# Optimization experiments

Measured on AMD Instinct MI355X. Metric: run time of the kernel, lower is better.

The kernel has to match this reference:

```python
import jax, jax.numpy as jnp
import numpy as np

ALPHA = 1.702  # gpt-oss gated-activation alpha
LIMIT = 7.0    # gpt-oss clamp limit
E, H, I = 8, 1024, 2048
B, S = 2, 2048


def setup_inputs() -> dict:
    key = jax.random.key(0)
    ks = jax.random.split(key, 6)
    return {
        "hidden_states": jax.random.normal(ks[0], (B, S, H), dtype=jnp.float32),
        "routing_weights": jax.random.uniform(ks[1], (B * S, E), dtype=jnp.float32),
        "gate_up_proj": jax.random.normal(ks[2], (E, H, 2 * I), dtype=jnp.float32) * 0.02,
        "gate_up_proj_bias": jax.random.normal(ks[3], (E, 2 * I), dtype=jnp.float32) * 0.02,
        "down_proj": jax.random.normal(ks[4], (E, I, H), dtype=jnp.float32) * 0.02,
        "down_proj_bias": jax.random.normal(ks[5], (E, H), dtype=jnp.float32) * 0.02,
    }


def reference(hidden_states, routing_weights, gate_up_proj, gate_up_proj_bias,
              down_proj, down_proj_bias):
    b, s, h = hidden_states.shape
    x = hidden_states.reshape(-1, h)  # [T, H]
    # all-experts dense path: [E, T, 2I]
    gate_up = jnp.einsum('th,ehd->etd', x, gate_up_proj) + gate_up_proj_bias[:, None, :]
    gate = gate_up[..., ::2]   # interleaved gate/up as in gpt-oss
    up = gate_up[..., 1::2]
    gate = jnp.minimum(gate, LIMIT)
    up = jnp.clip(up, -LIMIT, LIMIT)
    glu = gate * jax.nn.sigmoid(gate * ALPHA)
    # [E, T, H]
    out_e = jnp.einsum('eti,eih->eth', (up + 1.0) * glu, down_proj) + down_proj_bias[:, None, :]
    # weighted sum over experts with routing weights [T, E]
    out = jnp.einsum('eth,te->th', out_e, routing_weights)
    return out.reshape(b, s, h)
```

## Files before the change

### kernel.cpp

```cpp
#include <hip/hip_runtime.h>
#include <cstdint>

#define E_  8
#define H_  1024
#define I_  2048
#define T_  4096
#define D2_ 4096
#define K2_ 16384

typedef __bf16 bf16x8 __attribute__((ext_vector_type(8)));
typedef float  f32x4  __attribute__((ext_vector_type(4)));

__device__ __forceinline__ unsigned short f2bf(float f) {
  unsigned int u = __float_as_uint(f);
  u += 0x7FFFu + ((u >> 16) & 1u);
  return (unsigned short)(u >> 16);
}

__device__ __forceinline__ void gll16(const void* g, void* l) {
  __builtin_amdgcn_global_load_lds(
      (const __attribute__((address_space(1))) unsigned int*)(uintptr_t)g,
      (__attribute__((address_space(3))) unsigned int*)(uintptr_t)l,
      16, 0, 0);
}

#define BARX()  __builtin_amdgcn_s_barrier()
#define FENCE() __builtin_amdgcn_sched_barrier(0)
#define WLG()   { asm volatile("s_waitcnt lgkmcnt(0)" ::: "memory"); __builtin_amdgcn_sched_barrier(0); }
#define LGK0()  asm volatile("s_waitcnt lgkmcnt(0)" ::: "memory")
#define WVM4()  asm volatile("s_waitcnt vmcnt(4)" ::: "memory")
#define WVM0()  asm volatile("s_waitcnt vmcnt(0)" ::: "memory")

__global__ void cast_x_kernel(const float* __restrict__ x,
                              unsigned short* __restrict__ xb) {
  const int idx = (blockIdx.x * 256 + threadIdx.x) * 8;
  float4 a = *(const float4*)(x + idx);
  float4 b = *(const float4*)(x + idx + 4);
  unsigned short o[8];
  o[0]=f2bf(a.x); o[1]=f2bf(a.y); o[2]=f2bf(a.z); o[3]=f2bf(a.w);
  o[4]=f2bf(b.x); o[5]=f2bf(b.y); o[6]=f2bf(b.z); o[7]=f2bf(b.w);
  *(uint4*)(xb + idx) = *(const uint4*)o;
}

__global__ void transp_w1_kernel(const float* __restrict__ gup,
                                 unsigned short* __restrict__ w1g,
                                 unsigned short* __restrict__ w1u) {
  __shared__ float tile[64][65];
  const int h0 = blockIdx.x * 64;
  const int d0 = blockIdx.y * 64;
  const int e  = blockIdx.z;
  const int tid = threadIdx.x;
  const int r  = tid >> 4;
  const int c4 = (tid & 15) * 4;
  const float* src = gup + ((size_t)e * H_ + h0) * D2_ + d0;
#pragma unroll
  for (int c = 0; c < 4; ++c) {
    const int row = r + 16 * c;
    float4 v = *(const float4*)(src + (size_t)row * D2_ + c4);
    tile[row][c4+0] = v.x; tile[row][c4+1] = v.y;
    tile[row][c4+2] = v.z; tile[row][c4+3] = v.w;
  }
  __syncthreads();
  const int hl = tid & 63;
  const int jg = tid >> 6;
  const size_t jbase = (size_t)e * I_ + (d0 >> 1);
#pragma unroll
  for (int jj = 0; jj < 8; ++jj) {
    const int jl = jg * 8 + jj;
    w1g[(jbase + jl) * H_ + h0 + hl] = f2bf(tile[hl][2*jl]);
    w1u[(jbase + jl) * H_ + h0 + hl] = f2bf(tile[hl][2*jl+1]);
  }
}

__global__ void transp_w2_kernel(const float* __restrict__ dp,
                                 unsigned short* __restrict__ w2t) {
  __shared__ float tile[64][65];
  const int k0 = blockIdx.x * 64;
  const int h0 = blockIdx.y * 64;
  const int tid = threadIdx.x;
  const int r  = tid >> 4;
  const int c4 = (tid & 15) * 4;
#pragma unroll
  for (int c = 0; c < 4; ++c) {
    const int row = r + 16 * c;
    float4 v = *(const float4*)(dp + (size_t)(k0 + row) * H_ + h0 + c4);
    tile[row][c4+0] = v.x; tile[row][c4+1] = v.y;
    tile[row][c4+2] = v.z; tile[row][c4+3] = v.w;
  }
  __syncthreads();
  const int kl = tid & 63;
  const int hg = tid >> 6;
#pragma unroll
  for (int hh = 0; hh < 16; ++hh) {
    const int hl = hg * 16 + hh;
    w2t[(size_t)(h0 + hl) * K2_ + k0 + kl] = f2bf(tile[kl][hl]);
  }
}


#define STA1(B, HF, KT) {                                                    \
  _Pragma("unroll")                                                           \
  for (int ld = 0; ld < 2; ++ld) {                                            \
    const int r = rA + (HF)*64 + ld*128;                                      \
    gll16(Ag + (size_t)r * H_ + (KT)*64 + sg, &lds[B][r*64 + sl]);            \
  } }
#define STG1(B, KT) {                                                         \
  _Pragma("unroll")                                                           \
  for (int ld = 0; ld < 2; ++ld) {                                            \
    const int r = rA + ld*64;                                                 \
    gll16(Gg + (size_t)r * H_ + (KT)*64 + sg, &lds[B][16384 + r*64 + sl]);    \
  } }
#define STU1(B, KT) {                                                         \
  _Pragma("unroll")                                                           \
  for (int ld = 0; ld < 2; ++ld) {                                            \
    const int r = rA + ld*64;                                                 \
    gll16(Ug + (size_t)r * H_ + (KT)*64 + sg, &lds[B][24576 + r*64 + sl]);    \
  } }
#define LDA1(B, MH) {                                                         \
  _Pragma("unroll")                                                           \
  for (int m = 0; m < 4; ++m) {                                               \
    const int ro = (wm*128 + (MH)*64 + m*16 + arow) * 64;                     \
    av[m][0] = *(const bf16x8*)&lds[B][ro + sw0];                             \
    av[m][1] = *(const bf16x8*)&lds[B][ro + sw1];                             \
  } }
#define LDB1(B, DST, BASE) {                                                  \
  _Pragma("unroll")                                                           \
  for (int n = 0; n < 2; ++n) {                                               \
    const int ro = (BASE) + (wn*32 + n*16 + arow) * 64;                       \
    DST[n][0] = *(const bf16x8*)&lds[B][ro + sw0];                            \
    DST[n][1] = *(const bf16x8*)&lds[B][ro + sw1];                            \
  } }
#define MMA1(ACC, MH, BV)                                                     \
  __builtin_amdgcn_s_setprio(1);                                              \
  _Pragma("unroll")                                                           \
  for (int m = 0; m < 4; ++m)                                                 \
  _Pragma("unroll")                                                           \
  for (int n = 0; n < 2; ++n) {                                               \
    ACC[(MH)*4+m][n] = __builtin_amdgcn_mfma_f32_16x16x32_bf16(av[m][0], BV[n][0], ACC[(MH)*4+m][n], 0,0,0); \
    ACC[(MH)*4+m][n] = __builtin_amdgcn_mfma_f32_16x16x32_bf16(av[m][1], BV[n][1], ACC[(MH)*4+m][n], 0,0,0); \
  }                                                                           \
  __builtin_amdgcn_s_setprio(0);

#define NT1 16
#define TILE1(B, U) {                                                         \
    \
  LDA1(B, 0); LDB1(B, bgv, 16384); LDB1(B, buv, 24576);                       \
  if ((U)+1 < NT1) { STA1((B)^1, 1, (U)+1); STG1((B)^1, (U)+1); }             \
  WLG();                                                                      \
  MMA1(accg, 0, bgv); MMA1(accu, 0, buv);                                     \
  BARX();                                                                     \
   \
  LDA1(B, 1);                                                                 \
  if ((U)+2 < NT1) { STA1(B, 0, (U)+2); STU1(B, (U)+2); }                     \
  WLG();                                                                      \
  MMA1(accu, 1, buv); MMA1(accg, 1, bgv);                                     \
  if ((U)+2 < NT1) { WVM4(); } else { WVM0(); }                               \
  BARX();                                                                     \
}

__global__ __launch_bounds__(512, 2) void gemm1_act_kernel(
    const unsigned short* __restrict__ xb,
    const unsigned short* __restrict__ w1g,
    const unsigned short* __restrict__ w1u,
    const float* __restrict__ gub,
    const float* __restrict__ rw,
    unsigned short* __restrict__ actW)
{
  __shared__ unsigned short lds[2][32768];
  const int tid  = threadIdx.x;
  const int lane = tid & 63;
  const int wv   = tid >> 6;
  const int wm   = wv >> 2;
  const int wn   = wv & 3;

  const int L  = blockIdx.x + 16 * blockIdx.y;
  const int xk = L & 7, xs = L >> 3;
  const int t0 = ((xk >> 1) * 4 + (xs & 3)) * 256;
  const int j0 = ((xk & 1) * 8 + (xs >> 2)) * 128;
  const int e  = blockIdx.z;

  const int arow = lane & 15;
  const int q    = lane >> 4;
  const int sw0  = ((q    ) ^ (arow & 7)) * 8;
  const int sw1  = ((q + 4) ^ (arow & 7)) * 8;
  const int sg   = ((tid & 7) ^ ((tid >> 3) & 7)) * 8;
  const int sl   = (tid & 7) * 8;
  const int rA   = tid >> 3;

  const unsigned short* Ag = xb  + (size_t)t0 * H_;
  const unsigned short* Gg = w1g + ((size_t)e * I_ + j0) * H_;
  const unsigned short* Ug = w1u + ((size_t)e * I_ + j0) * H_;

  const f32x4 zero = {0.f, 0.f, 0.f, 0.f};
  f32x4 accg[8][2], accu[8][2];
#pragma unroll
  for (int m = 0; m < 8; ++m)
#pragma unroll
    for (int n = 0; n < 2; ++n) { accg[m][n] = zero; accu[m][n] = zero; }
  bf16x8 av[4][2], bgv[2][2], buv[2][2];

  STA1(0, 0, 0); STU1(0, 0); STA1(0, 1, 0); STG1(0, 0);
  STA1(1, 0, 1); STU1(1, 1);
  WVM4(); BARX();

#pragma unroll 1
  for (int u = 0; u < NT1; u += 2) {
    TILE1(0, u);
    TILE1(1, u+1);
  }

  const float* gbE = gub + (size_t)e * D2_;
#pragma unroll
  for (int n = 0; n < 2; ++n) {
    const int j = j0 + wn*32 + n*16 + arow;
    const float2 bgu = *(const float2*)&gbE[2*j];
#pragma unroll
    for (int mf = 0; mf < 8; ++mf) {
#pragma unroll
      for (int ri = 0; ri < 4; ++ri) {
        const int tt = t0 + wm*128 + mf*16 + q*4 + ri;
        float g = accg[mf][n][ri] + bgu.x;
        float u2 = accu[mf][n][ri] + bgu.y;
        g  = fminf(g, 7.0f);
        u2 = fminf(fmaxf(u2, -7.0f), 7.0f);
        const float s   = 1.0f / (1.0f + __expf(-1.702f * g));
        const float val = (u2 + 1.0f) * (g * s) * rw[tt * 8 + e];
        actW[(size_t)tt * K2_ + e * I_ + j] = f2bf(val);
      }
    }
  }
}


#define STA2(B, HF, KT) {                                                    \
  _Pragma("unroll")                                                           \
  for (int ld = 0; ld < 2; ++ld) {                                            \
    const int r = rA + (HF)*64 + ld*128;                                      \
    gll16(Ag + (size_t)r * K2_ + (KT)*64 + sg, &lds[B][r*64 + sl]);           \
  } }
#define STB2(B, NH, KT) {                                                    \
  _Pragma("unroll")                                                           \
  for (int ld = 0; ld < 2; ++ld) {                                            \
    const int lr = rA + ld*64;                                                \
    const int r  = (lr & 31) + (NH)*32 + ((lr >> 5) << 6);                    \
    gll16(Bgp + (size_t)r * K2_ + (KT)*64 + sg, &lds[B][16384 + r*64 + sl]);  \
  } }
#define LDA2(B, MH) {                                                         \
  _Pragma("unroll")                                                           \
  for (int m = 0; m < 4; ++m) {                                               \
    const int ro = (wm*128 + (MH)*64 + m*16 + arow) * 64;                     \
    av[m][0] = *(const bf16x8*)&lds[B][ro + sw0];                             \
    av[m][1] = *(const bf16x8*)&lds[B][ro + sw1];                             \
  } }
#define LDB2(B, DST, NH) {                                                   \
  _Pragma("unroll")                                                           \
  for (int n = 0; n < 2; ++n) {                                               \
    const int ro = 16384 + (wn*64 + (NH)*32 + n*16 + arow) * 64;              \
    DST[n][0] = *(const bf16x8*)&lds[B][ro + sw0];                            \
    DST[n][1] = *(const bf16x8*)&lds[B][ro + sw1];                            \
  } }
#define MMA2(MH, NH, BV)                                                      \
  __builtin_amdgcn_s_setprio(1);                                              \
  _Pragma("unroll")                                                           \
  for (int m = 0; m < 4; ++m)                                                 \
  _Pragma("unroll")                                                           \
  for (int n = 0; n < 2; ++n) {                                               \
    acc[(MH)*4+m][(NH)*2+n] = __builtin_amdgcn_mfma_f32_16x16x32_bf16(av[m][0], BV[n][0], acc[(MH)*4+m][(NH)*2+n], 0,0,0); \
    acc[(MH)*4+m][(NH)*2+n] = __builtin_amdgcn_mfma_f32_16x16x32_bf16(av[m][1], BV[n][1], acc[(MH)*4+m][(NH)*2+n], 0,0,0); \
  }                                                                           \
  __builtin_amdgcn_s_setprio(0);

#define NT2 64
#define TILE2(B, U) {                                                         \
  if ((U)+1 < NT2) { STA2((B)^1, 0, (U)+1); STA2((B)^1, 1, (U)+1);            \
                     STB2((B)^1, 0, (U)+1); STB2((B)^1, 1, (U)+1); }          \
  FENCE();                                                                    \
  LDA2(B, 0); LDB2(B, bv0, 0); LDB2(B, bv1, 1);                               \
  MMA2(0, 0, bv0); MMA2(0, 1, bv1);                                           \
  LDA2(B, 1);                                                                 \
  MMA2(1, 0, bv0); MMA2(1, 1, bv1);                                           \
  LGK0();                                                                     \
  if ((U)+1 < NT2) WVM0();                                                    \
  BARX();                                                                     \
  FENCE();                                                                    \
}

__global__ __launch_bounds__(512, 2) void gemm2_kernel(
    const unsigned short* __restrict__ actW,
    const unsigned short* __restrict__ w2t,
    float* __restrict__ part)
{
  __shared__ unsigned short lds[2][32768];
  const int tid  = threadIdx.x;
  const int lane = tid & 63;
  const int wv   = tid >> 6;
  const int wm   = wv >> 2;
  const int wn   = wv & 3;

  const int L  = blockIdx.x + 16 * (blockIdx.y + 4 * blockIdx.z);
  const int xk = L & 7, xs = L >> 3;
  const int t0 = ((xk & 1) * 8 + (xs & 7)) * 256;
  const int h0 = (xs >> 3) * 256;
  const int cz = xk >> 1;
  const int c0 = cz * 4096;

  const int arow = lane & 15;
  const int q    = lane >> 4;
  const int sw0  = ((q    ) ^ (arow & 7)) * 8;
  const int sw1  = ((q + 4) ^ (arow & 7)) * 8;
  const int sg   = ((tid & 7) ^ ((tid >> 3) & 7)) * 8;
  const int sl   = (tid & 7) * 8;
  const int rA   = tid >> 3;

  const unsigned short* Ag  = actW + (size_t)t0 * K2_ + c0;
  const unsigned short* Bgp = w2t  + (size_t)h0 * K2_ + c0;

  const f32x4 zero = {0.f, 0.f, 0.f, 0.f};
  f32x4 acc[8][4];
#pragma unroll
  for (int m = 0; m < 8; ++m)
#pragma unroll
    for (int n = 0; n < 4; ++n) acc[m][n] = zero;
  bf16x8 av[4][2], bv0[2][2], bv1[2][2];

  STA2(0, 0, 0); STA2(0, 1, 0); STB2(0, 0, 0); STB2(0, 1, 0);
  WVM0(); BARX(); FENCE();

#pragma unroll 1
  for (int u = 0; u < NT2; u += 2) {
    TILE2(0, u);
    TILE2(1, u+1);
  }

  float* P = part + (size_t)cz * ((size_t)T_ * H_);
#pragma unroll
  for (int mf = 0; mf < 8; ++mf)
#pragma unroll
    for (int nf = 0; nf < 4; ++nf)
#pragma unroll
      for (int ri = 0; ri < 4; ++ri) {
        const int tt = t0 + wm*128 + mf*16 + q*4 + ri;
        const int h  = h0 + wn*64 + nf*16 + arow;
        P[(size_t)tt * H_ + h] = acc[mf][nf][ri];
      }
}

__global__ void reduce_kernel(const float* __restrict__ part,
                              const float* __restrict__ rw,
                              const float* __restrict__ dpb,
                              float* __restrict__ out) {
  const int idx = blockIdx.x * 256 + threadIdx.x;
  const int t  = idx >> 8;
  const int hq = idx & 255;
  const float4* p = (const float4*)part;
  float4 v = p[idx];
  float4 a;
  a = p[idx + 1048576]; v.x += a.x; v.y += a.y; v.z += a.z; v.w += a.w;
  a = p[idx + 2097152]; v.x += a.x; v.y += a.y; v.z += a.z; v.w += a.w;
  a = p[idx + 3145728]; v.x += a.x; v.y += a.y; v.z += a.z; v.w += a.w;
  const float4 w0 = *(const float4*)(rw + t*8);
  const float4 w1 = *(const float4*)(rw + t*8 + 4);
  const float wgt[8] = {w0.x, w0.y, w0.z, w0.w, w1.x, w1.y, w1.z, w1.w};
  const float4* db = (const float4*)dpb;
#pragma unroll
  for (int e2 = 0; e2 < 8; ++e2) {
    float4 b = db[e2*256 + hq];
    v.x += wgt[e2]*b.x; v.y += wgt[e2]*b.y; v.z += wgt[e2]*b.z; v.w += wgt[e2]*b.w;
  }
  ((float4*)out)[idx] = v;
}

extern "C" void kernel_launch(void* const* d_in, const int* in_sizes, int n_in,
                              void* d_out, int out_size, void* d_ws, size_t ws_size,
                              hipStream_t stream) {
  const float* hs  = (const float*)d_in[0];
  const float* rw  = (const float*)d_in[1];
  const float* gup = (const float*)d_in[2];
  const float* gub = (const float*)d_in[3];
  const float* dp  = (const float*)d_in[4];
  const float* dpb = (const float*)d_in[5];
  float* out = (float*)d_out;

  char* ws = (char*)d_ws;
  unsigned short* xb   = (unsigned short*)(ws);
  unsigned short* w1g  = (unsigned short*)(ws + 8388608);
  unsigned short* w1u  = (unsigned short*)(ws + 41943040);
  float*          part = (float*)(ws + 8388608);
  unsigned short* w2t  = (unsigned short*)(ws + 75497472);
  unsigned short* actW = (unsigned short*)(ws + 109051904);

  hipLaunchKernelGGL(cast_x_kernel, dim3((T_ * H_) / 2048), dim3(256), 0, stream, hs, xb);
  hipLaunchKernelGGL(transp_w1_kernel, dim3(H_/64, D2_/64, E_), dim3(256), 0, stream, gup, w1g, w1u);
  hipLaunchKernelGGL(transp_w2_kernel, dim3(K2_/64, H_/64), dim3(256), 0, stream, dp, w2t);
  hipLaunchKernelGGL(gemm1_act_kernel, dim3(T_/256, I_/128, E_), dim3(512), 0, stream,
                     xb, w1g, w1u, gub, rw, actW);
  hipLaunchKernelGGL(gemm2_kernel, dim3(T_/256, H_/256, 4), dim3(512), 0, stream,
                     actW, w2t, part);
  hipLaunchKernelGGL(reduce_kernel, dim3((T_ * H_ / 4) / 256), dim3(256), 0, stream,
                     part, rw, dpb, out);
}
```

Baseline: 455.6 us.

## Interleave gate/up weight rows in 16-row groups and simplify gemm1 pipeline

The weight transpose now writes gate and up rows into a single packed buffer, interleaved in groups of 16, so gemm1 loads one contiguous B tile instead of two separate gate and up tiles. The gemm1 main loop is rewritten to prefetch the whole next K tile at once and run one barrier per tile, with a single accumulator array whose column pairs hold gate and up. This cuts the number of separate load streams and barriers. The trade-off is a simpler double-buffer scheme that waits for all loads (vmcnt 0) each tile, which may expose more memory latency.

```diff
diff --git a/kernel.cpp b/kernel.cpp
--- a/kernel.cpp
+++ b/kernel.cpp
@@ -26,9 +26,7 @@
 
 #define BARX()  __builtin_amdgcn_s_barrier()
 #define FENCE() __builtin_amdgcn_sched_barrier(0)
-#define WLG()   { asm volatile("s_waitcnt lgkmcnt(0)" ::: "memory"); __builtin_amdgcn_sched_barrier(0); }
 #define LGK0()  asm volatile("s_waitcnt lgkmcnt(0)" ::: "memory")
-#define WVM4()  asm volatile("s_waitcnt vmcnt(4)" ::: "memory")
 #define WVM0()  asm volatile("s_waitcnt vmcnt(0)" ::: "memory")
 
 __global__ void cast_x_kernel(const float* __restrict__ x,
@@ -43,8 +41,7 @@
 }
 
 __global__ void transp_w1_kernel(const float* __restrict__ gup,
-                                 unsigned short* __restrict__ w1g,
-                                 unsigned short* __restrict__ w1u) {
+                                 unsigned short* __restrict__ w1p) {
   __shared__ float tile[64][65];
   const int h0 = blockIdx.x * 64;
   const int d0 = blockIdx.y * 64;
@@ -63,12 +60,14 @@
   __syncthreads();
   const int hl = tid & 63;
   const int jg = tid >> 6;
-  const size_t jbase = (size_t)e * I_ + (d0 >> 1);
 #pragma unroll
   for (int jj = 0; jj < 8; ++jj) {
     const int jl = jg * 8 + jj;
-    w1g[(jbase + jl) * H_ + h0 + hl] = f2bf(tile[hl][2*jl]);
-    w1u[(jbase + jl) * H_ + h0 + hl] = f2bf(tile[hl][2*jl+1]);
+    const int jE = (d0 >> 1) + jl;
+    const size_t Rg = (size_t)((jE >> 4) * 32 + (jE & 15));
+    const size_t base = (size_t)e * 4096;
+    w1p[(base + Rg     ) * H_ + h0 + hl] = f2bf(tile[hl][2*jl]);
+    w1p[(base + Rg + 16) * H_ + h0 + hl] = f2bf(tile[hl][2*jl+1]);
   }
 }
 
@@ -98,23 +97,20 @@
 }
 
 
+#define NT1 16
+
 #define STA1(B, HF, KT) {                                                    \
   _Pragma("unroll")                                                           \
   for (int ld = 0; ld < 2; ++ld) {                                            \
     const int r = rA + (HF)*64 + ld*128;                                      \
     gll16(Ag + (size_t)r * H_ + (KT)*64 + sg, &lds[B][r*64 + sl]);            \
   } }
-#define STG1(B, KT) {                                                         \
+#define STB1(B, NH, KT) {                                                    \
   _Pragma("unroll")                                                           \
   for (int ld = 0; ld < 2; ++ld) {                                            \
-    const int r = rA + ld*64;                                                 \
-    gll16(Gg + (size_t)r * H_ + (KT)*64 + sg, &lds[B][16384 + r*64 + sl]);    \
-  } }
-#define STU1(B, KT) {                                                         \
-  _Pragma("unroll")                                                           \
-  for (int ld = 0; ld < 2; ++ld) {                                            \
-    const int r = rA + ld*64;                                                 \
-    gll16(Ug + (size_t)r * H_ + (KT)*64 + sg, &lds[B][24576 + r*64 + sl]);    \
+    const int lr = rA + ld*64;                                                \
+    const int r  = (lr & 31) + (NH)*32 + ((lr >> 5) << 6);                    \
+    gll16(Bgp + (size_t)r * H_ + (KT)*64 + sg, &lds[B][16384 + r*64 + sl]);   \
   } }
 #define LDA1(B, MH) {                                                         \
   _Pragma("unroll")                                                           \
@@ -123,45 +119,41 @@
     av[m][0] = *(const bf16x8*)&lds[B][ro + sw0];                             \
     av[m][1] = *(const bf16x8*)&lds[B][ro + sw1];                             \
   } }
-#define LDB1(B, DST, BASE) {                                                  \
+#define LDB1(B, DST, NH) {                                                    \
   _Pragma("unroll")                                                           \
   for (int n = 0; n < 2; ++n) {                                               \
-    const int ro = (BASE) + (wn*32 + n*16 + arow) * 64;                       \
+    const int ro = 16384 + (wn*64 + (NH)*32 + n*16 + arow) * 64;              \
     DST[n][0] = *(const bf16x8*)&lds[B][ro + sw0];                            \
     DST[n][1] = *(const bf16x8*)&lds[B][ro + sw1];                            \
   } }
-#define MMA1(ACC, MH, BV)                                                     \
+#define MMA1(MH, NH, BV)                                                      \
   __builtin_amdgcn_s_setprio(1);                                              \
   _Pragma("unroll")                                                           \
   for (int m = 0; m < 4; ++m)                                                 \
   _Pragma("unroll")                                                           \
   for (int n = 0; n < 2; ++n) {                                               \
-    ACC[(MH)*4+m][n] = __builtin_amdgcn_mfma_f32_16x16x32_bf16(av[m][0], BV[n][0], ACC[(MH)*4+m][n], 0,0,0); \
-    ACC[(MH)*4+m][n] = __builtin_amdgcn_mfma_f32_16x16x32_bf16(av[m][1], BV[n][1], ACC[(MH)*4+m][n], 0,0,0); \
+    acc[(MH)*4+m][(NH)*2+n] = __builtin_amdgcn_mfma_f32_16x16x32_bf16(av[m][0], BV[n][0], acc[(MH)*4+m][(NH)*2+n], 0,0,0); \
+    acc[(MH)*4+m][(NH)*2+n] = __builtin_amdgcn_mfma_f32_16x16x32_bf16(av[m][1], BV[n][1], acc[(MH)*4+m][(NH)*2+n], 0,0,0); \
   }                                                                           \
   __builtin_amdgcn_s_setprio(0);
 
-#define NT1 16
 #define TILE1(B, U) {                                                         \
-    \
-  LDA1(B, 0); LDB1(B, bgv, 16384); LDB1(B, buv, 24576);                       \
-  if ((U)+1 < NT1) { STA1((B)^1, 1, (U)+1); STG1((B)^1, (U)+1); }             \
-  WLG();                                                                      \
-  MMA1(accg, 0, bgv); MMA1(accu, 0, buv);                                     \
+  if ((U)+1 < NT1) { STA1((B)^1, 0, (U)+1); STA1((B)^1, 1, (U)+1);            \
+                     STB1((B)^1, 0, (U)+1); STB1((B)^1, 1, (U)+1); }          \
+  FENCE();                                                                    \
+  LDA1(B, 0); LDB1(B, bv0, 0); LDB1(B, bv1, 1);                               \
+  MMA1(0, 0, bv0); MMA1(0, 1, bv1);                                           \
+  LDA1(B, 1);                                                                 \
+  MMA1(1, 0, bv0); MMA1(1, 1, bv1);                                           \
+  LGK0();                                                                     \
+  if ((U)+1 < NT1) WVM0();                                                    \
   BARX();                                                                     \
-   \
-  LDA1(B, 1);                                                                 \
-  if ((U)+2 < NT1) { STA1(B, 0, (U)+2); STU1(B, (U)+2); }                     \
-  WLG();                                                                      \
-  MMA1(accu, 1, buv); MMA1(accg, 1, bgv);                                     \
-  if ((U)+2 < NT1) { WVM4(); } else { WVM0(); }                               \
-  BARX();                                                                     \
+  FENCE();                                                                    \
 }
 
 __global__ __launch_bounds__(512, 2) void gemm1_act_kernel(
     const unsigned short* __restrict__ xb,
-    const unsigned short* __restrict__ w1g,
-    const unsigned short* __restrict__ w1u,
+    const unsigned short* __restrict__ w1p,
     const float* __restrict__ gub,
     const float* __restrict__ rw,
     unsigned short* __restrict__ actW)
@@ -187,21 +179,19 @@
   const int sl   = (tid & 7) * 8;
   const int rA   = tid >> 3;
 
-  const unsigned short* Ag = xb  + (size_t)t0 * H_;
-  const unsigned short* Gg = w1g + ((size_t)e * I_ + j0) * H_;
-  const unsigned short* Ug = w1u + ((size_t)e * I_ + j0) * H_;
+  const unsigned short* Ag  = xb + (size_t)t0 * H_;
+  const unsigned short* Bgp = w1p + ((size_t)e * 4096 + 2 * j0) * H_;
 
   const f32x4 zero = {0.f, 0.f, 0.f, 0.f};
-  f32x4 accg[8][2], accu[8][2];
+  f32x4 acc[8][4];
 #pragma unroll
   for (int m = 0; m < 8; ++m)
 #pragma unroll
-    for (int n = 0; n < 2; ++n) { accg[m][n] = zero; accu[m][n] = zero; }
-  bf16x8 av[4][2], bgv[2][2], buv[2][2];
-
-  STA1(0, 0, 0); STU1(0, 0); STA1(0, 1, 0); STG1(0, 0);
-  STA1(1, 0, 1); STU1(1, 1);
-  WVM4(); BARX();
+    for (int n = 0; n < 4; ++n) acc[m][n] = zero;
+  bf16x8 av[4][2], bv0[2][2], bv1[2][2];
+
+  STA1(0, 0, 0); STA1(0, 1, 0); STB1(0, 0, 0); STB1(0, 1, 0);
+  WVM0(); BARX(); FENCE();
 
 #pragma unroll 1
   for (int u = 0; u < NT1; u += 2) {
@@ -211,16 +201,16 @@
 
   const float* gbE = gub + (size_t)e * D2_;
 #pragma unroll
-  for (int n = 0; n < 2; ++n) {
-    const int j = j0 + wn*32 + n*16 + arow;
+  for (int p = 0; p < 2; ++p) {
+    const int j = j0 + (wn*2 + p)*16 + arow;
     const float2 bgu = *(const float2*)&gbE[2*j];
 #pragma unroll
     for (int mf = 0; mf < 8; ++mf) {
 #pragma unroll
       for (int ri = 0; ri < 4; ++ri) {
         const int tt = t0 + wm*128 + mf*16 + q*4 + ri;
-        float g = accg[mf][n][ri] + bgu.x;
-        float u2 = accu[mf][n][ri] + bgu.y;
+        float g  = acc[mf][2*p  ][ri] + bgu.x;
+        float u2 = acc[mf][2*p+1][ri] + bgu.y;
         g  = fminf(g, 7.0f);
         u2 = fminf(fmaxf(u2, -7.0f), 7.0f);
         const float s   = 1.0f / (1.0f + __expf(-1.702f * g));
@@ -383,17 +373,16 @@
 
   char* ws = (char*)d_ws;
   unsigned short* xb   = (unsigned short*)(ws);
-  unsigned short* w1g  = (unsigned short*)(ws + 8388608);
-  unsigned short* w1u  = (unsigned short*)(ws + 41943040);
+  unsigned short* w1p  = (unsigned short*)(ws + 8388608);
   float*          part = (float*)(ws + 8388608);
   unsigned short* w2t  = (unsigned short*)(ws + 75497472);
   unsigned short* actW = (unsigned short*)(ws + 109051904);
 
   hipLaunchKernelGGL(cast_x_kernel, dim3((T_ * H_) / 2048), dim3(256), 0, stream, hs, xb);
-  hipLaunchKernelGGL(transp_w1_kernel, dim3(H_/64, D2_/64, E_), dim3(256), 0, stream, gup, w1g, w1u);
+  hipLaunchKernelGGL(transp_w1_kernel, dim3(H_/64, D2_/64, E_), dim3(256), 0, stream, gup, w1p);
   hipLaunchKernelGGL(transp_w2_kernel, dim3(K2_/64, H_/64), dim3(256), 0, stream, dp, w2t);
-  hipLaunchKernelGGL(gemm1_act_kernel, dim3(T_/256, I_/128, E_), dim3(512), 0, stream,
-                     xb, w1g, w1u, gub, rw, actW);
+  hipLaunchKernelGGL(gemm1_act_kernel, dim3(16, 16, E_), dim3(512), 0, stream,
+                     xb, w1p, gub, rw, actW);
   hipLaunchKernelGGL(gemm2_kernel, dim3(T_/256, H_/256, 4), dim3(512), 0, stream,
                      actW, w2t, part);
   hipLaunchKernelGGL(reduce_kernel, dim3((T_ * H_ / 4) / 256), dim3(256), 0, stream,
```

Measured after the change: 450.9 us, median of 2. Within noise of the previous version (-1.0%).
